# Performance work log

Hardware: AMD Instinct MI355X
Metric: run time of the kernel (lower is better)

The kernel has to match this reference:

```python
import jax, jax.numpy as jnp
import numpy as np

N = 50000      # nodes in current tree level
N_CH = 3       # actual children present in mailbox
D = 4          # max_output_degree
H = 256        # h_size


def setup_inputs() -> dict:
    key = jax.random.key(0)
    ks = jax.random.split(key, 6)
    return {
        "neighbour_h": jax.random.normal(ks[0], (N, N_CH, H), dtype=jnp.float32),
        "neighbour_c": jax.random.normal(ks[1], (N, N_CH, H), dtype=jnp.float32),
        "f_input": jax.random.normal(ks[2], (N, H), dtype=jnp.float32),
        "iou_input": jax.random.normal(ks[3], (N, 3 * H), dtype=jnp.float32),
        # torch nn.Linear convention: weight [out, in]; one per child position
        "U_f": jax.random.normal(ks[4], (D, H, H), dtype=jnp.float32) * 0.05,
        "U_iou": jax.random.normal(ks[5], (D, 3 * H, H), dtype=jnp.float32) * 0.05,
    }


def reference(neighbour_h, neighbour_c, f_input, iou_input, U_f, U_iou):
    n, n_ch, h = neighbour_h.shape
    d = U_f.shape[0]
    pad = d - n_ch
    # check_missing_children: pad with bottom_h / bottom_c == zeros
    nh = jnp.pad(neighbour_h, ((0, 0), (0, pad), (0, 0)))  # [N, D, H]
    nc = jnp.pad(neighbour_c, ((0, 0), (0, pad), (0, 0)))  # [N, D, H]
    # per-position forget gates: U_f_i @ h_i, plus f_input repeated per child
    f_logits = jnp.einsum('ndh,dkh->ndk', nh, U_f) + f_input[:, None, :]
    # iou gate (canonical n-ary tree-LSTM): sum_i U_iou_i @ h_i, plus iou_input
    iou_aggr = jnp.einsum('ndh,dkh->nk', nh, U_iou) + iou_input  # [N, 3H]
    f = jax.nn.sigmoid(f_logits)
    c_aggr = jnp.sum(f * nc, axis=1)  # [N, H]
    # apply_node_func: iou = iou_input + iou_aggr (iou_input counted twice, as in source)
    iou = iou_input + iou_aggr
    i, o, u = jnp.split(iou, 3, axis=1)
    c = jax.nn.sigmoid(i) * jnp.tanh(u) + c_aggr
    h_out = jax.nn.sigmoid(o) * jnp.tanh(c)
    return (h_out, c)
```

## Files before the change

kernel.cpp:

```cpp
#include <hip/hip_runtime.h>
#include <cstdint>
#include <cstddef>

#define NNODES 50000
#define HD 256
#define NCH 3
#define BM 32

typedef __attribute__((ext_vector_type(8))) short shortx8;
typedef __attribute__((ext_vector_type(4))) float floatx4;

__device__ __forceinline__ unsigned short f2bf(float x) {
    union { float f; uint32_t u; } v; v.f = x;
    uint32_t r = v.u + 0x7fffu + ((v.u >> 16) & 1u);
    return (unsigned short)(r >> 16);
}
__device__ __forceinline__ shortx8 cvt8(float4 a, float4 b) {
    shortx8 o;
    o[0] = (short)f2bf(a.x); o[1] = (short)f2bf(a.y);
    o[2] = (short)f2bf(a.z); o[3] = (short)f2bf(a.w);
    o[4] = (short)f2bf(b.x); o[5] = (short)f2bf(b.y);
    o[6] = (short)f2bf(b.z); o[7] = (short)f2bf(b.w);
    return o;
}
__device__ __forceinline__ float sigf(float x) {
    return 1.0f / (1.0f + __expf(-x));
}
__device__ __forceinline__ float tanhfast(float x) {
    return 1.0f - 2.0f / (__expf(2.0f * x) + 1.0f);
}
__device__ __forceinline__ floatx4 mfma16(shortx8 a, shortx8 b, floatx4 c) {
    return __builtin_amdgcn_mfma_f32_16x16x32_bf16(a, b, c, 0, 0, 0);
}

__global__ void prep_weights(const float* __restrict__ U_f,
                             const float* __restrict__ U_iou,
                             unsigned short* __restrict__ wsB) {
    int idx = blockIdx.x * 256 + threadIdx.x;
    int lane = idx & 63;
    int ks   = (idx >> 6) & 7;
    int tile = (idx >> 9) & 63;
    int d    = idx >> 15;
    if (d >= NCH) return;
    int col = tile * 16 + (lane & 15);
    int k0  = ks * 32 + (lane >> 4) * 8;
    const float* src = (col < 256)
        ? (U_f   + (((size_t)d * 256 + col)         * 256 + k0))
        : (U_iou + (((size_t)d * 768 + (col - 256)) * 256 + k0));
    shortx8 o;
    #pragma unroll
    for (int e = 0; e < 8; ++e) o[e] = (short)f2bf(src[e]);
    reinterpret_cast<shortx8*>(wsB)[idx] = o;
}

__global__ __launch_bounds__(512, 4) void treelstm_main(
    const float* __restrict__ nh,
    const float* __restrict__ ncc,
    const float* __restrict__ f_in,
    const float* __restrict__ iou_in,
    const unsigned short* __restrict__ wsB,
    float* __restrict__ out)
{
    __shared__ unsigned short sA[NCH * BM * 32 * 8];

    const int tid  = threadIdx.x;
    const int nb   = blockIdx.x * BM;
    const int lane = tid & 63;
    const int w    = tid >> 6;
    const int cl   = lane & 15;
    const int g    = lane >> 4;

    const shortx8* Bfr = reinterpret_cast<const shortx8*>(wsB);

    #pragma unroll
    for (int i = 0; i < 6; ++i) {
        int c    = i * 512 + tid;
        int d    = c >> 10;
        int node = (c >> 5) & 31;
        int slot = c & 31;
        int gn   = nb + node;
        shortx8 o;
        if (gn < NNODES) {
            const float4* q = reinterpret_cast<const float4*>(
                nh + ((size_t)gn * (NCH * HD) + d * HD + slot * 8));
            o = cvt8(q[0], q[1]);
        } else {
            #pragma unroll
            for (int e = 0; e < 8; ++e) o[e] = 0;
        }
        int idx = (d * BM + node) * 32 + (slot ^ (node & 7));
        *reinterpret_cast<shortx8*>(&sA[idx * 8]) = o;
    }
    __syncthreads();

    const int  n0  = nb + cl;
    const int  n1  = nb + 16 + cl;
    const bool v1  = (n1 < NNODES);
    const int  n1c = v1 ? n1 : n0;

    const int c0 = w * 32 + g * 4;
    floatx4 fin[2][2];
    fin[0][0] = *reinterpret_cast<const floatx4*>(f_in + (size_t)n0  * HD + c0);
    fin[1][0] = *reinterpret_cast<const floatx4*>(f_in + (size_t)n0  * HD + c0 + 16);
    fin[0][1] = *reinterpret_cast<const floatx4*>(f_in + (size_t)n1c * HD + c0);
    fin[1][1] = *reinterpret_cast<const floatx4*>(f_in + (size_t)n1c * HD + c0 + 16);

    floatx4 cagg[2][2];
    floatx4 accIOU[3][2][2];
    #pragma unroll
    for (int j = 0; j < 2; ++j)
        #pragma unroll
        for (int nt = 0; nt < 2; ++nt) {
            #pragma unroll
            for (int r = 0; r < 4; ++r) cagg[j][nt][r] = 0.0f;
            #pragma unroll
            for (int s = 0; s < 3; ++s)
                #pragma unroll
                for (int r = 0; r < 4; ++r) accIOU[s][j][nt][r] = 0.0f;
        }

    const int xr = cl & 7;

    #pragma unroll 1
    for (int d = 0; d < NCH; ++d) {
        floatx4 ncr[2][2];
        ncr[0][0] = *reinterpret_cast<const floatx4*>(
            ncc + (size_t)n0  * (NCH * HD) + d * HD + c0);
        ncr[1][0] = *reinterpret_cast<const floatx4*>(
            ncc + (size_t)n0  * (NCH * HD) + d * HD + c0 + 16);
        ncr[0][1] = *reinterpret_cast<const floatx4*>(
            ncc + (size_t)n1c * (NCH * HD) + d * HD + c0);
        ncr[1][1] = *reinterpret_cast<const floatx4*>(
            ncc + (size_t)n1c * (NCH * HD) + d * HD + c0 + 16);

        floatx4 accF[2][2];
        #pragma unroll
        for (int j = 0; j < 2; ++j)
            #pragma unroll
            for (int nt = 0; nt < 2; ++nt)
                #pragma unroll
                for (int r = 0; r < 4; ++r) accF[j][nt][r] = 0.0f;

        #pragma unroll 2
        for (int ks = 0; ks < 8; ++ks) {
            shortx8 a0 = Bfr[((d * 64 + 2 * w)     * 8 + ks) * 64 + lane];
            shortx8 a1 = Bfr[((d * 64 + 2 * w + 1) * 8 + ks) * 64 + lane];
            int sl = (ks * 4 + g) ^ xr;
            shortx8 b0 = *reinterpret_cast<const shortx8*>(
                &sA[((d * BM + cl)      * 32 + sl) * 8]);
            shortx8 b1 = *reinterpret_cast<const shortx8*>(
                &sA[((d * BM + 16 + cl) * 32 + sl) * 8]);
            accF[0][0] = mfma16(a0, b0, accF[0][0]);
            accF[0][1] = mfma16(a0, b1, accF[0][1]);
            accF[1][0] = mfma16(a1, b0, accF[1][0]);
            accF[1][1] = mfma16(a1, b1, accF[1][1]);
        }
        #pragma unroll
        for (int j = 0; j < 2; ++j)
            #pragma unroll
            for (int nt = 0; nt < 2; ++nt)
                #pragma unroll
                for (int r = 0; r < 4; ++r)
                    cagg[j][nt][r] +=
                        sigf(accF[j][nt][r] + fin[j][nt][r]) * ncr[j][nt][r];

        #pragma unroll
        for (int s = 0; s < 3; ++s) {
            #pragma unroll 2
            for (int ks = 0; ks < 8; ++ks) {
                shortx8 a0 = Bfr[((d * 64 + 16 + s * 16 + 2 * w)     * 8 + ks) * 64 + lane];
                shortx8 a1 = Bfr[((d * 64 + 16 + s * 16 + 2 * w + 1) * 8 + ks) * 64 + lane];
                int sl = (ks * 4 + g) ^ xr;
                shortx8 b0 = *reinterpret_cast<const shortx8*>(
                    &sA[((d * BM + cl)      * 32 + sl) * 8]);
                shortx8 b1 = *reinterpret_cast<const shortx8*>(
                    &sA[((d * BM + 16 + cl) * 32 + sl) * 8]);
                accIOU[s][0][0] = mfma16(a0, b0, accIOU[s][0][0]);
                accIOU[s][0][1] = mfma16(a0, b1, accIOU[s][0][1]);
                accIOU[s][1][0] = mfma16(a1, b0, accIOU[s][1][0]);
                accIOU[s][1][1] = mfma16(a1, b1, accIOU[s][1][1]);
            }
        }
    }

    #pragma unroll
    for (int nt = 0; nt < 2; ++nt) {
        if (nt == 1 && !v1) continue;
        int n = (nt == 0) ? n0 : n1;
        #pragma unroll
        for (int j = 0; j < 2; ++j) {
            int col = c0 + j * 16;
            size_t base = (size_t)n * 768 + col;
            floatx4 i4 = *reinterpret_cast<const floatx4*>(iou_in + base);
            floatx4 o4 = *reinterpret_cast<const floatx4*>(iou_in + base + 256);
            floatx4 u4 = *reinterpret_cast<const floatx4*>(iou_in + base + 512);
            floatx4 cc, hh;
            #pragma unroll
            for (int r = 0; r < 4; ++r) {
                float iv = accIOU[0][j][nt][r] + 2.0f * i4[r];
                float ov = accIOU[1][j][nt][r] + 2.0f * o4[r];
                float uv = accIOU[2][j][nt][r] + 2.0f * u4[r];
                float c  = sigf(iv) * tanhfast(uv) + cagg[j][nt][r];
                cc[r] = c;
                hh[r] = sigf(ov) * tanhfast(c);
            }
            *reinterpret_cast<floatx4*>(out + (size_t)n * HD + col) = hh;
            *reinterpret_cast<floatx4*>(out + (size_t)(NNODES + n) * HD + col) = cc;
        }
    }
}

extern "C" void kernel_launch(void* const* d_in, const int* in_sizes, int n_in,
                              void* d_out, int out_size, void* d_ws, size_t ws_size,
                              hipStream_t stream) {
    const float* nh     = (const float*)d_in[0];
    const float* ncc    = (const float*)d_in[1];
    const float* f_in   = (const float*)d_in[2];
    const float* iou_in = (const float*)d_in[3];
    const float* U_f    = (const float*)d_in[4];
    const float* U_iou  = (const float*)d_in[5];
    unsigned short* wsB = (unsigned short*)d_ws;

    if (ws_size < (size_t)(3 * 64 * 8 * 64) * 16) return;

    hipLaunchKernelGGL(prep_weights, dim3(384), dim3(256), 0, stream,
                       U_f, U_iou, wsB);
    hipLaunchKernelGGL(treelstm_main, dim3((NNODES + BM - 1) / BM), dim3(512),
                       0, stream, nh, ncc, f_in, iou_in, wsB, (float*)d_out);
}
```

Baseline: 342.3 us.

## Switch to 32x32x16 bf16 MFMA and fuse forget and IOU gate loops

```diff
diff --git a/kernel.cpp b/kernel.cpp
--- a/kernel.cpp
+++ b/kernel.cpp
@@ -9,11 +9,15 @@
 
 typedef __attribute__((ext_vector_type(8))) short shortx8;
 typedef __attribute__((ext_vector_type(4))) float floatx4;
+typedef __attribute__((ext_vector_type(16))) float floatx16;
 
 __device__ __forceinline__ unsigned short f2bf(float x) {
     union { float f; uint32_t u; } v; v.f = x;
     uint32_t r = v.u + 0x7fffu + ((v.u >> 16) & 1u);
     return (unsigned short)(r >> 16);
+}
+__device__ __forceinline__ float bf2f(unsigned short u) {
+    union { uint32_t u; float f; } v; v.u = ((uint32_t)u) << 16; return v.f;
 }
 __device__ __forceinline__ shortx8 cvt8(float4 a, float4 b) {
     shortx8 o;
@@ -29,21 +33,21 @@
 __device__ __forceinline__ float tanhfast(float x) {
     return 1.0f - 2.0f / (__expf(2.0f * x) + 1.0f);
 }
-__device__ __forceinline__ floatx4 mfma16(shortx8 a, shortx8 b, floatx4 c) {
-    return __builtin_amdgcn_mfma_f32_16x16x32_bf16(a, b, c, 0, 0, 0);
+__device__ __forceinline__ floatx16 mfma32(shortx8 a, shortx8 b, floatx16 c) {
+    return __builtin_amdgcn_mfma_f32_32x32x16_bf16(a, b, c, 0, 0, 0);
 }
 
-__global__ void prep_weights(const float* __restrict__ U_f,
-                             const float* __restrict__ U_iou,
-                             unsigned short* __restrict__ wsB) {
+__global__ void prep_weights32(const float* __restrict__ U_f,
+                               const float* __restrict__ U_iou,
+                               unsigned short* __restrict__ wsB) {
     int idx = blockIdx.x * 256 + threadIdx.x;
     int lane = idx & 63;
-    int ks   = (idx >> 6) & 7;
-    int tile = (idx >> 9) & 63;
+    int ks   = (idx >> 6) & 15;
+    int tile = (idx >> 10) & 31;
     int d    = idx >> 15;
     if (d >= NCH) return;
-    int col = tile * 16 + (lane & 15);
-    int k0  = ks * 32 + (lane >> 4) * 8;
+    int col = tile * 32 + (lane & 31);
+    int k0  = ks * 16 + (lane >> 5) * 8;
     const float* src = (col < 256)
         ? (U_f   + (((size_t)d * 256 + col)         * 256 + k0))
         : (U_iou + (((size_t)d * 768 + (col - 256)) * 256 + k0));
@@ -66,9 +70,10 @@
     const int tid  = threadIdx.x;
     const int nb   = blockIdx.x * BM;
     const int lane = tid & 63;
-    const int w    = tid >> 6;
-    const int cl   = lane & 15;
-    const int g    = lane >> 4;
+    const int cg   = tid >> 6;
+    const int nl   = lane & 31;
+    const int hi   = lane >> 5;
+    const int colb = cg * 32 + hi * 4;
 
     const shortx8* Bfr = reinterpret_cast<const shortx8*>(wsB);
 
@@ -93,103 +98,64 @@
     }
     __syncthreads();
 
-    const int  n0  = nb + cl;
-    const int  n1  = nb + 16 + cl;
-    const bool v1  = (n1 < NNODES);
-    const int  n1c = v1 ? n1 : n0;
+    const int  n     = nb + nl;
+    const bool valid = (n < NNODES);
+    const int  nc_   = valid ? n : (NNODES - 1);
 
-    const int c0 = w * 32 + g * 4;
-    floatx4 fin[2][2];
-    fin[0][0] = *reinterpret_cast<const floatx4*>(f_in + (size_t)n0  * HD + c0);
-    fin[1][0] = *reinterpret_cast<const floatx4*>(f_in + (size_t)n0  * HD + c0 + 16);
-    fin[0][1] = *reinterpret_cast<const floatx4*>(f_in + (size_t)n1c * HD + c0);
-    fin[1][1] = *reinterpret_cast<const floatx4*>(f_in + (size_t)n1c * HD + c0 + 16);
+    ushort4 finb[4];
+    #pragma unroll
+    for (int q = 0; q < 4; ++q) {
+        floatx4 v = *reinterpret_cast<const floatx4*>(
+            f_in + (size_t)nc_ * HD + colb + q * 8);
+        finb[q] = ushort4{f2bf(v[0]), f2bf(v[1]), f2bf(v[2]), f2bf(v[3])};
+    }
 
-    floatx4 cagg[2][2];
-    floatx4 accIOU[3][2][2];
+    float cagg[16];
     #pragma unroll
-    for (int j = 0; j < 2; ++j)
-        #pragma unroll
-        for (int nt = 0; nt < 2; ++nt) {
-            #pragma unroll
-            for (int r = 0; r < 4; ++r) cagg[j][nt][r] = 0.0f;
-            #pragma unroll
-            for (int s = 0; s < 3; ++s)
-                #pragma unroll
-                for (int r = 0; r < 4; ++r) accIOU[s][j][nt][r] = 0.0f;
-        }
+    for (int t = 0; t < 16; ++t) cagg[t] = 0.0f;
 
-    const int xr = cl & 7;
+    floatx16 accI, accO, accU;
+    #pragma unroll
+    for (int t = 0; t < 16; ++t) { accI[t] = 0.0f; accO[t] = 0.0f; accU[t] = 0.0f; }
+
+    const int nsw = nl & 7;
 
     #pragma unroll 1
     for (int d = 0; d < NCH; ++d) {
-        floatx4 ncr[2][2];
-        ncr[0][0] = *reinterpret_cast<const floatx4*>(
-            ncc + (size_t)n0  * (NCH * HD) + d * HD + c0);
-        ncr[1][0] = *reinterpret_cast<const floatx4*>(
-            ncc + (size_t)n0  * (NCH * HD) + d * HD + c0 + 16);
-        ncr[0][1] = *reinterpret_cast<const floatx4*>(
-            ncc + (size_t)n1c * (NCH * HD) + d * HD + c0);
-        ncr[1][1] = *reinterpret_cast<const floatx4*>(
-            ncc + (size_t)n1c * (NCH * HD) + d * HD + c0 + 16);
-
-        floatx4 accF[2][2];
+        floatx16 accF;
         #pragma unroll
-        for (int j = 0; j < 2; ++j)
-            #pragma unroll
-            for (int nt = 0; nt < 2; ++nt)
-                #pragma unroll
-                for (int r = 0; r < 4; ++r) accF[j][nt][r] = 0.0f;
+        for (int t = 0; t < 16; ++t) accF[t] = 0.0f;
 
         #pragma unroll 2
-        for (int ks = 0; ks < 8; ++ks) {
-            shortx8 a0 = Bfr[((d * 64 + 2 * w)     * 8 + ks) * 64 + lane];
-            shortx8 a1 = Bfr[((d * 64 + 2 * w + 1) * 8 + ks) * 64 + lane];
-            int sl = (ks * 4 + g) ^ xr;
-            shortx8 b0 = *reinterpret_cast<const shortx8*>(
-                &sA[((d * BM + cl)      * 32 + sl) * 8]);
-            shortx8 b1 = *reinterpret_cast<const shortx8*>(
-                &sA[((d * BM + 16 + cl) * 32 + sl) * 8]);
-            accF[0][0] = mfma16(a0, b0, accF[0][0]);
-            accF[0][1] = mfma16(a0, b1, accF[0][1]);
-            accF[1][0] = mfma16(a1, b0, accF[1][0]);
-            accF[1][1] = mfma16(a1, b1, accF[1][1]);
+        for (int ks = 0; ks < 16; ++ks) {
+            shortx8 aF = Bfr[((d * 32 +      cg) * 16 + ks) * 64 + lane];
+            shortx8 aI = Bfr[((d * 32 +  8 + cg) * 16 + ks) * 64 + lane];
+            shortx8 aO = Bfr[((d * 32 + 16 + cg) * 16 + ks) * 64 + lane];
+            shortx8 aU = Bfr[((d * 32 + 24 + cg) * 16 + ks) * 64 + lane];
+            int ch = (ks * 2 + hi) ^ nsw;
+            shortx8 b = *reinterpret_cast<const shortx8*>(
+                &sA[((d * BM + nl) * 32 + ch) * 8]);
+            accF = mfma32(aF, b, accF);
+            accI = mfma32(aI, b, accI);
+            accO = mfma32(aO, b, accO);
+            accU = mfma32(aU, b, accU);
         }
-        #pragma unroll
-        for (int j = 0; j < 2; ++j)
-            #pragma unroll
-            for (int nt = 0; nt < 2; ++nt)
-                #pragma unroll
-                for (int r = 0; r < 4; ++r)
-                    cagg[j][nt][r] +=
-                        sigf(accF[j][nt][r] + fin[j][nt][r]) * ncr[j][nt][r];
 
         #pragma unroll
-        for (int s = 0; s < 3; ++s) {
-            #pragma unroll 2
-            for (int ks = 0; ks < 8; ++ks) {
-                shortx8 a0 = Bfr[((d * 64 + 16 + s * 16 + 2 * w)     * 8 + ks) * 64 + lane];
-                shortx8 a1 = Bfr[((d * 64 + 16 + s * 16 + 2 * w + 1) * 8 + ks) * 64 + lane];
-                int sl = (ks * 4 + g) ^ xr;
-                shortx8 b0 = *reinterpret_cast<const shortx8*>(
-                    &sA[((d * BM + cl)      * 32 + sl) * 8]);
-                shortx8 b1 = *reinterpret_cast<const shortx8*>(
-                    &sA[((d * BM + 16 + cl) * 32 + sl) * 8]);
-                accIOU[s][0][0] = mfma16(a0, b0, accIOU[s][0][0]);
-                accIOU[s][0][1] = mfma16(a0, b1, accIOU[s][0][1]);
-                accIOU[s][1][0] = mfma16(a1, b0, accIOU[s][1][0]);
-                accIOU[s][1][1] = mfma16(a1, b1, accIOU[s][1][1]);
-            }
+        for (int q = 0; q < 4; ++q) {
+            floatx4 ncr = *reinterpret_cast<const floatx4*>(
+                ncc + (size_t)nc_ * (NCH * HD) + d * HD + colb + q * 8);
+            cagg[q * 4 + 0] += sigf(accF[q * 4 + 0] + bf2f(finb[q].x)) * ncr[0];
+            cagg[q * 4 + 1] += sigf(accF[q * 4 + 1] + bf2f(finb[q].y)) * ncr[1];
+            cagg[q * 4 + 2] += sigf(accF[q * 4 + 2] + bf2f(finb[q].z)) * ncr[2];
+            cagg[q * 4 + 3] += sigf(accF[q * 4 + 3] + bf2f(finb[q].w)) * ncr[3];
         }
     }
 
-    #pragma unroll
-    for (int nt = 0; nt < 2; ++nt) {
-        if (nt == 1 && !v1) continue;
-        int n = (nt == 0) ? n0 : n1;
+    if (valid) {
         #pragma unroll
-        for (int j = 0; j < 2; ++j) {
-            int col = c0 + j * 16;
+        for (int q = 0; q < 4; ++q) {
+            int col = colb + q * 8;
             size_t base = (size_t)n * 768 + col;
             floatx4 i4 = *reinterpret_cast<const floatx4*>(iou_in + base);
             floatx4 o4 = *reinterpret_cast<const floatx4*>(iou_in + base + 256);
@@ -197,10 +163,11 @@
             floatx4 cc, hh;
             #pragma unroll
             for (int r = 0; r < 4; ++r) {
-                float iv = accIOU[0][j][nt][r] + 2.0f * i4[r];
-                float ov = accIOU[1][j][nt][r] + 2.0f * o4[r];
-                float uv = accIOU[2][j][nt][r] + 2.0f * u4[r];
-                float c  = sigf(iv) * tanhfast(uv) + cagg[j][nt][r];
+                int t = q * 4 + r;
+                float iv = accI[t] + 2.0f * i4[r];
+                float ov = accO[t] + 2.0f * o4[r];
+                float uv = accU[t] + 2.0f * u4[r];
+                float c  = sigf(iv) * tanhfast(uv) + cagg[t];
                 cc[r] = c;
                 hh[r] = sigf(ov) * tanhfast(c);
             }
@@ -221,9 +188,9 @@
     const float* U_iou  = (const float*)d_in[5];
     unsigned short* wsB = (unsigned short*)d_ws;
 
-    if (ws_size < (size_t)(3 * 64 * 8 * 64) * 16) return;
+    if (ws_size < (size_t)(3 * 32 * 16 * 64) * 16) return;
 
-    hipLaunchKernelGGL(prep_weights, dim3(384), dim3(256), 0, stream,
+    hipLaunchKernelGGL(prep_weights32, dim3(384), dim3(256), 0, stream,
                        U_f, U_iou, wsB);
     hipLaunchKernelGGL(treelstm_main, dim3((NNODES + BM - 1) / BM), dim3(512),
                        0, stream, nh, ncc, f_in, iou_in, wsB, (float*)d_out);
```

New measurement: 283.5 us. -17.2%, faster.
